# Performance work log

Hardware: AMD Instinct MI355X
Metric: run time of the kernel (lower is better)

## Reference

```python
import jax, jax.numpy as jnp
import numpy as np

# BQQ block dims: Y_sign (p,j,k,m,l), Z_sign (p,j,k,l,n); in=k*n=4096, out=j*m=4096
P, J, K, M, L, N = 2, 32, 32, 128, 16, 128
ACT_BITS = 8  # activation quantization bits


def setup_inputs() -> dict:
    key = jax.random.key(0)
    ks = jax.random.split(key, 7)
    x = jax.random.normal(ks[0], (1, 512, K * N), dtype=jnp.float32)
    # sign matrices in {-1,+1}
    Y_sign = jnp.where(jax.random.normal(ks[1], (P, J, K, M, L)) >= 0, 1.0, -1.0).astype(jnp.float32)
    Z_sign = jnp.where(jax.random.normal(ks[2], (P, J, K, L, N)) >= 0, 1.0, -1.0).astype(jnp.float32)
    # per-block positive scales (abs-mean in the original, so strictly > 0)
    Y_scale = jax.random.uniform(ks[3], (P, J, K, 1, 1), minval=0.01, maxval=0.1, dtype=jnp.float32)
    Z_scale = jax.random.uniform(ks[4], (P, J, K, 1, 1), minval=0.01, maxval=0.1, dtype=jnp.float32)
    A = jax.random.normal(ks[5], (P, J, K, 4), dtype=jnp.float32) * 0.1
    bias = jax.random.normal(ks[6], (J * M,), dtype=jnp.float32) * 0.1
    return {"input": x, "Y_sign": Y_sign, "Z_sign": Z_sign,
            "Y_scale": Y_scale, "Z_scale": Z_scale, "A": A, "bias": bias}


def reference(input, Y_sign, Z_sign, Y_scale, Z_scale, A, bias):
    # --- activation quantization (act_bits = 8, simple round, no STE) ---
    qmax = float(2 ** (ACT_BITS - 1) - 1)  # 127
    x_max = jnp.max(input)
    x_min = jnp.min(input)
    act_scale = jnp.maximum((x_max - x_min) / (2.0 * qmax), 1e-8)
    X = jnp.clip(jnp.round(input / act_scale), -qmax, qmax) * act_scale

    # --- dequantize sign * scale ---
    Y_q = Y_sign * Y_scale  # (p,j,k,m,l)
    Z_q = Z_sign * Z_scale  # (p,j,k,l,n)

    orig_shape = X.shape[:-1]
    X_kn = X.reshape(-1, K, N)  # (B,k,n)

    # chained block einsums
    T = jnp.einsum('bkn,pjkln->bpjkl', X_kn, Z_q)          # (B,p,j,k,l)
    core = jnp.einsum('pjkml,bpjkl->bpjkm', Y_q, T)        # (B,p,j,k,m)

    # quant_bias=True correction terms: A[...,0..3] = (a,b,c,d)
    out1 = jnp.einsum('bpjkm,pjk->bjm', core, A[..., 0])

    Y_sum = Y_q.sum(axis=-1)                               # (p,j,k,m)
    B_coef = jnp.einsum('pjk,pjkm->jkm', A[..., 1], Y_sum)
    Sx = X_kn.sum(axis=-1)                                 # (B,k)
    out2 = jnp.einsum('bk,jkm->bjm', Sx, B_coef)

    Zs = Z_q.sum(axis=-2)                                  # (p,j,k,n)
    Tz = jnp.einsum('bkn,pjkn->bpjk', X_kn, Zs)
    out3 = jnp.einsum('bpjk,pjk->bj', Tz, A[..., 2])

    D_coef = A[..., 3].sum(axis=0)                         # (j,k)
    out4 = jnp.einsum('bk,jk->bj', Sx, D_coef)

    out_bjm = out1 + out2 + (out3 + out4)[:, :, None]      # (B,j,m)
    out_2d = out_bjm.reshape(-1, J * M) + bias
    return out_2d.reshape(*orig_shape, J * M)
```

## Files before the change

### kernel.cpp

```cpp
#include <hip/hip_runtime.h>
#include <hip/hip_bf16.h>

typedef __attribute__((ext_vector_type(4))) float f32x4;
typedef __attribute__((ext_vector_type(8))) short bf16x8;
typedef __attribute__((ext_vector_type(4))) unsigned int u32x4;

#define GLOBAL_AS __attribute__((address_space(1)))
#define LDS_AS __attribute__((address_space(3)))

static __device__ __forceinline__ unsigned short f2bf(float f) {
  __hip_bfloat16 h = __float2bfloat16(f);
  return __builtin_bit_cast(unsigned short, h);
}
static __device__ __forceinline__ float bf2f(unsigned short u) {
  unsigned int v = ((unsigned int)u) << 16;
  return __builtin_bit_cast(float, v);
}
static __device__ __forceinline__ void load_lds16(const void* g, void* l) {
  __builtin_amdgcn_global_load_lds((GLOBAL_AS void*)g, (LDS_AS void*)l, 16, 0, 0);
}

__global__ __launch_bounds__(256) void k_minmax_part(const float* __restrict__ x,
                                                     float* __restrict__ part) {
  int tid = blockIdx.x * 256 + threadIdx.x;
  const float4* xv = (const float4*)x;
  float mn = 3.4e38f, mx = -3.4e38f;
#pragma unroll
  for (int rep = 0; rep < 8; ++rep) {
    float4 v = xv[tid + rep * 65536];
    mn = fminf(mn, fminf(fminf(v.x, v.y), fminf(v.z, v.w)));
    mx = fmaxf(mx, fmaxf(fmaxf(v.x, v.y), fmaxf(v.z, v.w)));
  }
#pragma unroll
  for (int o = 32; o > 0; o >>= 1) {
    mn = fminf(mn, __shfl_down(mn, o));
    mx = fmaxf(mx, __shfl_down(mx, o));
  }
  __shared__ float smn[4], smx[4];
  int lane = threadIdx.x & 63, w = threadIdx.x >> 6;
  if (lane == 0) { smn[w] = mn; smx[w] = mx; }
  __syncthreads();
  if (threadIdx.x == 0) {
    mn = fminf(fminf(smn[0], smn[1]), fminf(smn[2], smn[3]));
    mx = fmaxf(fmaxf(smx[0], smx[1]), fmaxf(smx[2], smx[3]));
    part[2 * blockIdx.x] = mn;
    part[2 * blockIdx.x + 1] = mx;
  }
}

__global__ __launch_bounds__(256) void k_fused(const float* __restrict__ x,
                                               const float* __restrict__ part,
                                               const float* __restrict__ Ysg,
                                               const float* __restrict__ Zsg,
                                               const float* __restrict__ Ysc,
                                               const float* __restrict__ Zsc,
                                               const float* __restrict__ Acoef,
                                               float* __restrict__ scl,
                                               unsigned short* __restrict__ xq,
                                               unsigned short* __restrict__ W) {
  const int t = threadIdx.x;
  if (blockIdx.x < 1024) {
    const int jk = blockIdx.x;
    __shared__ unsigned short Yb[2 * 128 * 24];
    __shared__ unsigned short Zb[128 * 36];
    __shared__ float B1p[2][128];
    __shared__ float C1[128];
    float cf0[2], cf2[2], cf4[2];
    float Dv;
    {
      float ys0 = Ysc[jk], zs0 = Zsc[jk], ys1 = Ysc[1024 + jk], zs1 = Zsc[1024 + jk];
      const float* A0p = Acoef + (size_t)jk * 4;
      const float* A1p = Acoef + (size_t)(1024 + jk) * 4;
      cf0[0] = A0p[0] * ys0 * zs0; cf0[1] = A1p[0] * ys1 * zs1;
      cf2[0] = A0p[1] * ys0;       cf2[1] = A1p[1] * ys1;
      cf4[0] = A0p[2] * zs0;       cf4[1] = A1p[2] * zs1;
      Dv = A0p[3] + A1p[3];
    }
#pragma unroll
    for (int rep = 0; rep < 4; ++rep) {
      int q = rep * 256 + t;
      int l0 = (q & 3) * 4, m = (q >> 2) & 127, p = q >> 9;
      float4 v = *(const float4*)(Ysg + (size_t)(p * 1024 + jk) * 2048 + m * 16 + l0);
      float s4 = v.x + v.y + v.z + v.w;
      s4 += __shfl_xor(s4, 1);
      s4 += __shfl_xor(s4, 2);
      if ((t & 3) == 0) B1p[p][m] = s4;
      float c0 = cf0[p];
      ushort4 o = make_ushort4(f2bf(c0 * v.x), f2bf(c0 * v.y), f2bf(c0 * v.z), f2bf(c0 * v.w));
      *(ushort4*)&Yb[(p * 128 + m) * 24 + l0] = o;
    }
#pragma unroll
    for (int rep = 0; rep < 4; ++rep) {
      int q = rep * 256 + t;
      int n0 = (q & 31) * 4, l = (q >> 5) & 15, p = q >> 9;
      float4 v = *(const float4*)(Zsg + (size_t)(p * 1024 + jk) * 2048 + l * 128 + n0);
      int pl = p * 16 + l;
      Zb[(n0 + 0) * 36 + pl] = f2bf(v.x);
      Zb[(n0 + 1) * 36 + pl] = f2bf(v.y);
      Zb[(n0 + 2) * 36 + pl] = f2bf(v.z);
      Zb[(n0 + 3) * 36 + pl] = f2bf(v.w);
    }
    __syncthreads();
    if (t < 128) {
      float s0 = 0.f, s1 = 0.f;
#pragma unroll
      for (int l = 0; l < 16; ++l) {
        s0 += bf2f(Zb[t * 36 + l]);
        s1 += bf2f(Zb[t * 36 + 16 + l]);
      }
      C1[t] = cf4[0] * s0 + cf4[1] * s1;
    }
    __syncthreads();
    const int lane = t & 63, wid = t >> 6;
    const int wm = wid >> 1, wn = wid & 1;
    const int grp = lane >> 4;
    bf16x8 af[4], bfr[4];
#pragma unroll
    for (int fm = 0; fm < 4; ++fm) {
      int m = wm * 64 + fm * 16 + (lane & 15);
      af[fm] = *(const bf16x8*)((const char*)Yb + ((grp >> 1) * 128 + m) * 48 + (grp & 1) * 16);
    }
#pragma unroll
    for (int fn = 0; fn < 4; ++fn) {
      int n = wn * 64 + fn * 16 + (lane & 15);
      const char* zp = (const char*)Zb + n * 72 + grp * 16;
      uint2 z0 = *(const uint2*)zp;
      uint2 z1 = *(const uint2*)(zp + 8);
      u32x4 zw; zw[0] = z0.x; zw[1] = z0.y; zw[2] = z1.x; zw[3] = z1.y;
      bfr[fn] = __builtin_bit_cast(bf16x8, zw);
    }
    f32x4 acc[4][4];
#pragma unroll
    for (int fm = 0; fm < 4; ++fm)
#pragma unroll
      for (int fn = 0; fn < 4; ++fn)
        acc[fm][fn] = __builtin_amdgcn_mfma_f32_16x16x32_bf16(af[fm], bfr[fn], (f32x4)(0.f), 0, 0, 0);
    const int j = jk >> 5, k = jk & 31;
    float c1v[4];
#pragma unroll
    for (int fn = 0; fn < 4; ++fn) c1v[fn] = C1[wn * 64 + fn * 16 + (lane & 15)];
#pragma unroll
    for (int fm = 0; fm < 4; ++fm) {
#pragma unroll
      for (int i = 0; i < 4; ++i) {
        int row = wm * 64 + fm * 16 + (grp)*4 + i;
        float b1v = cf2[0] * B1p[0][row] + cf2[1] * B1p[1][row] + Dv;
        size_t rowoff = (size_t)(j * 128 + row) * 4096 + (size_t)(k * 128);
#pragma unroll
        for (int fn = 0; fn < 4; ++fn) {
          int col = wn * 64 + fn * 16 + (lane & 15);
          W[rowoff + col] = f2bf(acc[fm][fn][i] + b1v + c1v[fn]);
        }
      }
    }
  } else {
    const int qb = blockIdx.x - 1024;
    float2 v2 = ((const float2*)part)[t];
    float mn = v2.x, mx = v2.y;
#pragma unroll
    for (int o = 32; o > 0; o >>= 1) {
      mn = fminf(mn, __shfl_down(mn, o));
      mx = fmaxf(mx, __shfl_down(mx, o));
    }
    __shared__ float smn2[4], smx2[4], ssc[1];
    int lane = t & 63, w = t >> 6;
    if (lane == 0) { smn2[w] = mn; smx2[w] = mx; }
    __syncthreads();
    if (t == 0) {
      mn = fminf(fminf(smn2[0], smn2[1]), fminf(smn2[2], smn2[3]));
      mx = fmaxf(fmaxf(smx2[0], smx2[1]), fmaxf(smx2[2], smx2[3]));
      ssc[0] = fmaxf((mx - mn) / 254.0f, 1e-8f);
      if (qb == 0) scl[0] = ssc[0];
    }
    __syncthreads();
    const float s = ssc[0];
    int i = qb * 256 + t;
    float4 v = ((const float4*)x)[i];
    float a = fminf(fmaxf(rintf(v.x / s), -127.f), 127.f);
    float b = fminf(fmaxf(rintf(v.y / s), -127.f), 127.f);
    float c = fminf(fmaxf(rintf(v.z / s), -127.f), 127.f);
    float d = fminf(fmaxf(rintf(v.w / s), -127.f), 127.f);
    ((ushort4*)xq)[i] = make_ushort4(f2bf(a), f2bf(b), f2bf(c), f2bf(d));
  }
}

__global__ __launch_bounds__(512) void k_gemm(const unsigned short* __restrict__ Xq,
                                              const unsigned short* __restrict__ W,
                                              float* __restrict__ out,
                                              unsigned short* __restrict__ P) {
  __shared__ unsigned short Al[2][256 * 64];
  __shared__ unsigned short Bl[2][256 * 64];
  const int t = threadIdx.x, lane = t & 63, wid = t >> 6;
  const int wg = (blockIdx.x & 7) * 32 + (blockIdx.x >> 3);
  const int bn = wg >> 4;
  const int sk = (wg >> 1) & 7;
  const int bm = wg & 1;
  const int wm = wid >> 2, wn = wid & 3;
  const int kbase = sk * 512;
  f32x4 acc[8][4];
#pragma unroll
  for (int a = 0; a < 8; ++a)
#pragma unroll
    for (int b = 0; b < 4; ++b) acc[a][b] = (f32x4)(0.f);

  const int lr = lane >> 3;
  const int lcb = (lane & 7) * 16;

  auto STAGE = [&](int buf, int kt) {
    const int k0 = kbase + kt * 64;
#pragma unroll
    for (int c = 0; c < 4; ++c) {
      int chunk = wid * 4 + c;
      int r = chunk * 8 + lr;
      int colb = lcb ^ ((r & 7) << 4);
      load_lds16(Xq + ((size_t)(bm * 256 + r) << 12) + k0 + (colb >> 1), &Al[buf][chunk * 512]);
    }
#pragma unroll
    for (int c = 0; c < 4; ++c) {
      int chunk = wid * 4 + c;
      int r = chunk * 8 + lr;
      int colb = lcb ^ ((r & 7) << 4);
      load_lds16(W + ((size_t)(bn * 256 + r) << 12) + k0 + (colb >> 1), &Bl[buf][chunk * 512]);
    }
  };

  auto COMPUTE = [&](int buf) {
#pragma unroll
    for (int ks = 0; ks < 2; ++ks) {
      bf16x8 af[8], bfr[4];
#pragma unroll
      for (int fm = 0; fm < 8; ++fm) {
        int r = wm * 128 + fm * 16 + (lane & 15);
        int colb = (ks * 64 + ((lane >> 4) * 16)) ^ ((r & 7) << 4);
        af[fm] = *(const bf16x8*)((const char*)&Al[buf][0] + r * 128 + colb);
      }
#pragma unroll
      for (int fn = 0; fn < 4; ++fn) {
        int r = wn * 64 + fn * 16 + (lane & 15);
        int colb = (ks * 64 + ((lane >> 4) * 16)) ^ ((r & 7) << 4);
        bfr[fn] = *(const bf16x8*)((const char*)&Bl[buf][0] + r * 128 + colb);
      }
#pragma unroll
      for (int fm = 0; fm < 8; ++fm)
#pragma unroll
        for (int fn = 0; fn < 4; ++fn)
          acc[fm][fn] = __builtin_amdgcn_mfma_f32_16x16x32_bf16(af[fm], bfr[fn], acc[fm][fn], 0, 0, 0);
    }
  };

  STAGE(0, 0);
  for (int it = 0; it < 8; ++it) {
    STAGE((it + 1) & 1, (it + 1) & 7);
    __builtin_amdgcn_sched_barrier(0);
    asm volatile("s_waitcnt vmcnt(8)" ::: "memory");
    __builtin_amdgcn_sched_barrier(0);
    __builtin_amdgcn_s_barrier();
    __builtin_amdgcn_sched_barrier(0);
    COMPUTE(it & 1);
    __builtin_amdgcn_sched_barrier(0);
    __builtin_amdgcn_s_barrier();
  }

  if (sk == 0) {
#pragma unroll
    for (int fn = 0; fn < 4; ++fn) {
      int col = bn * 256 + wn * 64 + fn * 16 + (lane & 15);
#pragma unroll
      for (int fm = 0; fm < 8; ++fm) {
#pragma unroll
        for (int i = 0; i < 4; ++i) {
          int row = bm * 256 + wm * 128 + fm * 16 + (lane >> 4) * 4 + i;
          out[(size_t)row * 4096 + col] = acc[fm][fn][i];
        }
      }
    }
  } else {
    unsigned short* Pk = P + (size_t)(sk - 1) * 2097152;
#pragma unroll
    for (int fn = 0; fn < 4; ++fn) {
      int col = bn * 256 + wn * 64 + fn * 16 + (lane & 15);
#pragma unroll
      for (int fm = 0; fm < 8; ++fm) {
#pragma unroll
        for (int i = 0; i < 4; ++i) {
          int row = bm * 256 + wm * 128 + fm * 16 + (lane >> 4) * 4 + i;
          Pk[(size_t)row * 4096 + col] = f2bf(acc[fm][fn][i]);
        }
      }
    }
  }
}

__global__ __launch_bounds__(256) void k_epi(float* __restrict__ out,
                                             const unsigned short* __restrict__ P,
                                             const float* __restrict__ scl,
                                             const float* __restrict__ bias) {
  int i4 = blockIdx.x * 256 + threadIdx.x;
  const float s = scl[0];
  float4 r = ((const float4*)out)[i4];
  float4 bv = ((const float4*)bias)[i4 & 1023];
  float sx = r.x, sy = r.y, sz = r.z, sw = r.w;
#pragma unroll
  for (int k = 0; k < 7; ++k) {
    ushort4 p = ((const ushort4*)(P + (size_t)k * 2097152))[i4];
    sx += bf2f(p.x); sy += bf2f(p.y); sz += bf2f(p.z); sw += bf2f(p.w);
  }
  ((float4*)out)[i4] = make_float4(sx * s + bv.x, sy * s + bv.y, sz * s + bv.z, sw * s + bv.w);
}

__global__ __launch_bounds__(512) void k_gemm_fb(const unsigned short* __restrict__ Xq,
                                                 const unsigned short* __restrict__ W,
                                                 const float* __restrict__ scl,
                                                 const float* __restrict__ bias,
                                                 float* __restrict__ out) {
  __shared__ unsigned short Al[4][128 * 64];
  __shared__ unsigned short Bl[4][64 * 64];
  const int t = threadIdx.x, lane = t & 63, wid = t >> 6;
  const int wg = (blockIdx.x & 7) * 32 + (blockIdx.x >> 3);
  const int bm = wg & 3;
  const int bn = wg >> 2;
  const int wm = wid >> 1, wn = wid & 1;
  f32x4 acc[2][2];
#pragma unroll
  for (int a = 0; a < 2; ++a)
#pragma unroll
    for (int b = 0; b < 2; ++b) acc[a][b] = (f32x4)(0.f);
  const int lr = lane >> 3;
  const int lcb = (lane & 7) * 16;
  auto STAGE = [&](int buf, int kt) {
    const int k0 = kt * 64;
#pragma unroll
    for (int c = 0; c < 2; ++c) {
      int chunk = wid * 2 + c;
      int r = chunk * 8 + lr;
      int colb = lcb ^ ((r & 7) << 4);
      load_lds16(Xq + ((size_t)(bm * 128 + r) << 12) + k0 + (colb >> 1), &Al[buf][chunk * 512]);
    }
    {
      int r = wid * 8 + lr;
      int colb = lcb ^ ((r & 7) << 4);
      load_lds16(W + ((size_t)(bn * 64 + r) << 12) + k0 + (colb >> 1), &Bl[buf][wid * 512]);
    }
  };
  auto COMPUTE = [&](int buf) {
#pragma unroll
    for (int ks = 0; ks < 2; ++ks) {
      bf16x8 af[2], bfr[2];
#pragma unroll
      for (int fm = 0; fm < 2; ++fm) {
        int r = wm * 32 + fm * 16 + (lane & 15);
        int colb = (ks * 64 + ((lane >> 4) * 16)) ^ ((r & 7) << 4);
        af[fm] = *(const bf16x8*)((const char*)&Al[buf][0] + r * 128 + colb);
      }
#pragma unroll
      for (int fn = 0; fn < 2; ++fn) {
        int r = wn * 32 + fn * 16 + (lane & 15);
        int colb = (ks * 64 + ((lane >> 4) * 16)) ^ ((r & 7) << 4);
        bfr[fn] = *(const bf16x8*)((const char*)&Bl[buf][0] + r * 128 + colb);
      }
#pragma unroll
      for (int fm = 0; fm < 2; ++fm)
#pragma unroll
        for (int fn = 0; fn < 2; ++fn)
          acc[fm][fn] = __builtin_amdgcn_mfma_f32_16x16x32_bf16(af[fm], bfr[fn], acc[fm][fn], 0, 0, 0);
    }
  };
  STAGE(0, 0); STAGE(1, 1); STAGE(2, 2);
  for (int t64 = 0; t64 < 64; ++t64) {
    STAGE((t64 + 3) & 3, (t64 + 3) & 63);
    __builtin_amdgcn_sched_barrier(0);
    asm volatile("s_waitcnt vmcnt(9)" ::: "memory");
    __builtin_amdgcn_sched_barrier(0);
    __builtin_amdgcn_s_barrier();
    __builtin_amdgcn_sched_barrier(0);
    COMPUTE(t64 & 3);
    __builtin_amdgcn_sched_barrier(0);
    __builtin_amdgcn_s_barrier();
  }
  const float s = scl[0];
#pragma unroll
  for (int fn = 0; fn < 2; ++fn) {
    int col = bn * 64 + wn * 32 + fn * 16 + (lane & 15);
    float bv = bias[col];
#pragma unroll
    for (int fm = 0; fm < 2; ++fm) {
#pragma unroll
      for (int i = 0; i < 4; ++i) {
        int row = bm * 128 + wm * 32 + fm * 16 + (lane >> 4) * 4 + i;
        out[(size_t)row * 4096 + col] = acc[fm][fn][i] * s + bv;
      }
    }
  }
}

extern "C" void kernel_launch(void* const* d_in, const int* in_sizes, int n_in,
                              void* d_out, int out_size, void* d_ws, size_t ws_size,
                              hipStream_t stream) {
  const float* x    = (const float*)d_in[0];
  const float* Ysg  = (const float*)d_in[1];
  const float* Zsg  = (const float*)d_in[2];
  const float* Ysc  = (const float*)d_in[3];
  const float* Zsc  = (const float*)d_in[4];
  const float* A    = (const float*)d_in[5];
  const float* bias = (const float*)d_in[6];
  float* out = (float*)d_out;

  char* ws = (char*)d_ws;
  float* scl  = (float*)ws;
  float* part = (float*)(ws + 256);
  unsigned short* Xq = (unsigned short*)(ws + 65536);
  unsigned short* W  = (unsigned short*)(ws + 65536 + (size_t)4194304);
  unsigned short* P  = (unsigned short*)(ws + 65536 + (size_t)4194304 + (size_t)33554432);

  k_minmax_part<<<dim3(256), dim3(256), 0, stream>>>(x, part);
  k_fused<<<dim3(3072), dim3(256), 0, stream>>>(x, part, Ysg, Zsg, Ysc, Zsc, A, scl, Xq, W);
  if (ws_size >= (size_t)65536 + 4194304 + 33554432 + 29360128) {
    k_gemm<<<dim3(256), dim3(512), 0, stream>>>(Xq, W, out, P);
    k_epi<<<dim3(2048), dim3(256), 0, stream>>>(out, P, scl, bias);
  } else {
    k_gemm_fb<<<dim3(256), dim3(512), 0, stream>>>(Xq, W, scl, bias, out);
  }
}
```

Before: 63.76 us.

## Store split-K partials in fragment-native layout and remap workgroup tiling

```diff
diff --git a/kernel.cpp b/kernel.cpp
--- a/kernel.cpp
+++ b/kernel.cpp
@@ -186,15 +186,14 @@
 
 __global__ __launch_bounds__(512) void k_gemm(const unsigned short* __restrict__ Xq,
                                               const unsigned short* __restrict__ W,
-                                              float* __restrict__ out,
                                               unsigned short* __restrict__ P) {
   __shared__ unsigned short Al[2][256 * 64];
   __shared__ unsigned short Bl[2][256 * 64];
   const int t = threadIdx.x, lane = t & 63, wid = t >> 6;
   const int wg = (blockIdx.x & 7) * 32 + (blockIdx.x >> 3);
-  const int bn = wg >> 4;
-  const int sk = (wg >> 1) & 7;
-  const int bm = wg & 1;
+  const int sk = wg >> 5;
+  const int bm = (wg >> 4) & 1;
+  const int bn = wg & 15;
   const int wm = wid >> 2, wn = wid & 3;
   const int kbase = sk * 512;
   f32x4 acc[8][4];
@@ -261,32 +260,16 @@
     __builtin_amdgcn_s_barrier();
   }
 
-  if (sk == 0) {
+  unsigned short* Pk = P + (size_t)sk * 2097152;
+  const int blkL = bm * 16 + bn;
+#pragma unroll
+  for (int fm = 0; fm < 8; ++fm) {
 #pragma unroll
     for (int fn = 0; fn < 4; ++fn) {
-      int col = bn * 256 + wn * 64 + fn * 16 + (lane & 15);
-#pragma unroll
-      for (int fm = 0; fm < 8; ++fm) {
-#pragma unroll
-        for (int i = 0; i < 4; ++i) {
-          int row = bm * 256 + wm * 128 + fm * 16 + (lane >> 4) * 4 + i;
-          out[(size_t)row * 4096 + col] = acc[fm][fn][i];
-        }
-      }
-    }
-  } else {
-    unsigned short* Pk = P + (size_t)(sk - 1) * 2097152;
-#pragma unroll
-    for (int fn = 0; fn < 4; ++fn) {
-      int col = bn * 256 + wn * 64 + fn * 16 + (lane & 15);
-#pragma unroll
-      for (int fm = 0; fm < 8; ++fm) {
-#pragma unroll
-        for (int i = 0; i < 4; ++i) {
-          int row = bm * 256 + wm * 128 + fm * 16 + (lane >> 4) * 4 + i;
-          Pk[(size_t)row * 4096 + col] = f2bf(acc[fm][fn][i]);
-        }
-      }
+      int idx = (((blkL * 8 + wid) * 32 + fm * 4 + fn) * 64) + lane;
+      ushort4 o = make_ushort4(f2bf(acc[fm][fn][0]), f2bf(acc[fm][fn][1]),
+                               f2bf(acc[fm][fn][2]), f2bf(acc[fm][fn][3]));
+      ((ushort4*)Pk)[idx] = o;
     }
   }
 }
@@ -295,17 +278,26 @@
                                              const unsigned short* __restrict__ P,
                                              const float* __restrict__ scl,
                                              const float* __restrict__ bias) {
-  int i4 = blockIdx.x * 256 + threadIdx.x;
+  int g = blockIdx.x * 256 + threadIdx.x;
+  const int lane = g & 63;
+  const int ff = (g >> 6) & 31;
+  const int fn = ff & 3, fm = ff >> 2;
+  const int wid = (g >> 11) & 7;
+  const int blkL = g >> 14;
+  const int bm = blkL >> 4, bn = blkL & 15;
+  const int wm = wid >> 2, wn = wid & 3;
+  const int row0 = bm * 256 + wm * 128 + fm * 16 + ((lane >> 4) << 2);
+  const int col = bn * 256 + wn * 64 + fn * 16 + (lane & 15);
   const float s = scl[0];
-  float4 r = ((const float4*)out)[i4];
-  float4 bv = ((const float4*)bias)[i4 & 1023];
-  float sx = r.x, sy = r.y, sz = r.z, sw = r.w;
-#pragma unroll
-  for (int k = 0; k < 7; ++k) {
-    ushort4 p = ((const ushort4*)(P + (size_t)k * 2097152))[i4];
-    sx += bf2f(p.x); sy += bf2f(p.y); sz += bf2f(p.z); sw += bf2f(p.w);
-  }
-  ((float4*)out)[i4] = make_float4(sx * s + bv.x, sy * s + bv.y, sz * s + bv.z, sw * s + bv.w);
+  const float bv = bias[col];
+  float sum[4] = {0.f, 0.f, 0.f, 0.f};
+#pragma unroll
+  for (int k = 0; k < 8; ++k) {
+    ushort4 p = ((const ushort4*)(P + (size_t)k * 2097152))[g];
+    sum[0] += bf2f(p.x); sum[1] += bf2f(p.y); sum[2] += bf2f(p.z); sum[3] += bf2f(p.w);
+  }
+#pragma unroll
+  for (int i = 0; i < 4; ++i) out[(size_t)(row0 + i) * 4096 + col] = sum[i] * s + bv;
 }
 
 __global__ __launch_bounds__(512) void k_gemm_fb(const unsigned short* __restrict__ Xq,
@@ -414,8 +406,8 @@
 
   k_minmax_part<<<dim3(256), dim3(256), 0, stream>>>(x, part);
   k_fused<<<dim3(3072), dim3(256), 0, stream>>>(x, part, Ysg, Zsg, Ysc, Zsc, A, scl, Xq, W);
-  if (ws_size >= (size_t)65536 + 4194304 + 33554432 + 29360128) {
-    k_gemm<<<dim3(256), dim3(512), 0, stream>>>(Xq, W, out, P);
+  if (ws_size >= (size_t)65536 + 4194304 + 33554432 + 33554432) {
+    k_gemm<<<dim3(256), dim3(512), 0, stream>>>(Xq, W, P);
     k_epi<<<dim3(2048), dim3(256), 0, stream>>>(out, P, scl, bias);
   } else {
     k_gemm_fb<<<dim3(256), dim3(512), 0, stream>>>(Xq, W, scl, bias, out);
```

Result: faster. 55.55 us (-12.9%).
